# Performance work log

Measured on AMD Instinct MI355X. Metric: run time of the kernel, lower is better.

The kernel has to match this reference:

```python
import jax, jax.numpy as jnp
import numpy as np

N = 50000      # nodes
E = 1600000    # edges (avg degree 32)
NF = 128       # hidden_nf
L = 4          # n_layers
EA = 1         # edge_attr_nf


def setup_inputs() -> dict:
    key = jax.random.key(0)
    ks = jax.random.split(key, 10)
    return {
        "pos": jax.random.normal(ks[0], (N, 3), jnp.float32),
        "v": jax.random.normal(ks[1], (N, 3), jnp.float32),
        "edge_attr": jax.random.normal(ks[2], (E, EA), jnp.float32),
        # phi: Linear(1+EA -> NF), SiLU, Linear(NF -> 1, no bias), Tanh
        "phi_w1": jax.random.normal(ks[3], (L, 1 + EA, NF), jnp.float32) * 0.1,
        "phi_b1": jnp.zeros((L, NF), jnp.float32),
        "phi_w2": jax.random.normal(ks[4], (L, NF, 1), jnp.float32) * 0.001,
        # coord_mlp_vel: Linear(1 -> NF), SiLU, Linear(NF -> 1)
        "vel_w1": jax.random.normal(ks[5], (L, 1, NF), jnp.float32) * 0.1,
        "vel_b1": jnp.zeros((L, NF), jnp.float32),
        "vel_w2": jax.random.normal(ks[6], (L, NF, 1), jnp.float32) * 0.1,
        "vel_b2": jnp.zeros((L, 1), jnp.float32),
        "edge_index": jax.random.randint(ks[7], (2, E), 0, N, dtype=jnp.int64),
    }


def _layer(x, vel_norm, v, row, col, edge_attr,
           pw1, pb1, pw2, vw1, vb1, vw2, vb2):
    # edge model: gather endpoints, radial feature, per-edge MLP
    x_diff = x[row] - x[col]                                        # [E,3]
    radial = jnp.sqrt(jnp.sum(x_diff * x_diff, axis=1, keepdims=True))  # [E,1]
    e_in = jnp.concatenate([radial, edge_attr], axis=1)             # [E,1+EA]
    h = jax.nn.silu(e_in @ pw1 + pb1)                               # [E,NF]
    e_out = jnp.tanh(h @ pw2)                                       # [E,1]
    m = x_diff * e_out                                              # [E,3]
    # node model: segment mean over receiving node (row)
    agg = jax.ops.segment_sum(m, row, num_segments=N)               # [N,3]
    cnt = jax.ops.segment_sum(jnp.ones((row.shape[0], 1), x.dtype), row,
                              num_segments=N)                        # [N,1]
    x = x + agg / jnp.maximum(cnt, 1.0)
    # velocity term: x += v * coord_mlp_vel(||v||)
    phi_v = jax.nn.silu(vel_norm @ vw1 + vb1) @ vw2 + vb2           # [N,1]
    return x + v * phi_v


def reference(pos, v, edge_attr, phi_w1, phi_b1, phi_w2,
              vel_w1, vel_b1, vel_w2, vel_b2, edge_index):
    row, col = edge_index[0], edge_index[1]
    vel_norm = jnp.sqrt(jnp.sum(v * v, axis=1, keepdims=True))      # [N,1]
    x = pos
    for i in range(L):
        x = _layer(x, vel_norm, v, row, col, edge_attr,
                   phi_w1[i], phi_b1[i], phi_w2[i],
                   vel_w1[i], vel_b1[i], vel_w2[i], vel_b2[i])
    return x
```

## Files before the change

### kernel.cpp

```cpp
#include <hip/hip_runtime.h>
#include <hip/hip_fp16.h>

#define NF 128
#define NL 4

#define NR 128
#define RMAXF 16.0f
#define NA 32
#define AMINF -8.0f
#define ARANGE 16.0f
#define AQMAX 511
#define NV 512
#define VMAXF 8.0f

#define BROWS_SHIFT 7
#define BROWS 128
#define NBMAX 512
#define BCAP 4480
#define EPT 16
#define EPB 4096

struct __align__(8) Half4 { __half2 lo; __half2 hi; };

__device__ __forceinline__ float fast_sigmoid(float x) {
    float z = __builtin_amdgcn_exp2f(-1.44269504f * x);
    return __builtin_amdgcn_rcpf(1.0f + z);
}
__device__ __forceinline__ float silu(float x) { return x * fast_sigmoid(x); }

__device__ __forceinline__ float fast_tanh(float x) {
    float y = fminf(fmaxf(x, -15.0f), 15.0f);
    float e2 = __builtin_amdgcn_exp2f(2.88539008f * y);
    return (e2 - 1.0f) * __builtin_amdgcn_rcpf(e2 + 1.0f);
}

__global__ __launch_bounds__(256) void setup1_kernel(
    const float* __restrict__ pw1, const float* __restrict__ pb1,
    const float* __restrict__ pw2, const float* __restrict__ vw1,
    const float* __restrict__ vb1, const float* __restrict__ vw2,
    const float* __restrict__ vb2,
    __half* __restrict__ etabh, float* __restrict__ vtab,
    int* __restrict__ counts, int* __restrict__ cursor)
{
    int t = blockIdx.x * 256 + threadIdx.x;
    if (t < NBMAX) counts[t] = 0;
    if (t == 0) *cursor = 0;

    if (t < NL * NR * NA) {
        int l = t / (NR * NA), rem = t - l * NR * NA;
        int ri = rem / NA, ai = rem - ri * NA;
        float r = ri * (RMAXF / (NR - 1));
        float a = AMINF + ai * (ARANGE / (NA - 1));
        const float* w1r = pw1 + l * 2 * NF;
        const float* w1a = w1r + NF;
        const float* b1  = pb1 + l * NF;
        const float* w2  = pw2 + l * NF;
        float acc = 0.f;
        #pragma unroll 8
        for (int k = 0; k < NF; ++k) {
            float pre = fmaf(r, w1r[k], fmaf(a, w1a[k], b1[k]));
            acc = fmaf(silu(pre), w2[k], acc);
        }
        etabh[t] = __float2half(fast_tanh(acc));
    } else if (t < NL * NR * NA + NL * NV) {
        int u = t - NL * NR * NA;
        int l = u / NV, vi = u - l * NV;
        float vn = vi * (VMAXF / (NV - 1));
        const float* w1 = vw1 + l * NF;
        const float* b1 = vb1 + l * NF;
        const float* w2 = vw2 + l * NF;
        float acc = 0.f;
        #pragma unroll 8
        for (int k = 0; k < NF; ++k) {
            float pre = fmaf(vn, w1[k], b1[k]);
            acc = fmaf(silu(pre), w2[k], acc);
        }
        vtab[u] = acc + vb2[l];
    }
}

__global__ __launch_bounds__(256) void passA_setup2_kernel(
    const int* __restrict__ row, const int* __restrict__ col,
    const float* __restrict__ ea, int* __restrict__ counts,
    unsigned int* __restrict__ coarse, int E, int gA,
    const __half* __restrict__ etabh, Half4* __restrict__ tab,
    const float* __restrict__ pos, const float* __restrict__ v,
    const float* __restrict__ vtab,
    float4* __restrict__ x4A, float4* __restrict__ v4,
    float* __restrict__ phv, int N)
{
    int tid = threadIdx.x;
    if ((int)blockIdx.x < gA) {
        __shared__ int hist[NBMAX];
        __shared__ int base[NBMAX];
        for (int i = tid; i < NBMAX; i += 256) hist[i] = 0;
        __syncthreads();
        int e0 = blockIdx.x * EPB;
        unsigned int rec[EPT];
        int bin[EPT];
        int rank[EPT];
        #pragma unroll
        for (int k = 0; k < EPT; ++k) {
            int e = e0 + k * 256 + tid;
            bin[k] = -1;
            if (e < E) {
                int r = row[e];
                int c = col[e];
                float a = fminf(fmaxf(ea[e], AMINF), AMINF + ARANGE);
                int aq = (int)fmaf(a - AMINF, (float)AQMAX / ARANGE, 0.5f);
                bin[k]  = r >> BROWS_SHIFT;
                rec[k]  = ((unsigned int)(r & (BROWS - 1)) << 25) |
                          ((unsigned int)c << 9) | (unsigned int)aq;
                rank[k] = atomicAdd(&hist[bin[k]], 1);
            }
        }
        __syncthreads();
        for (int i = tid; i < NBMAX; i += 256) {
            int h = hist[i];
            base[i] = (h > 0) ? atomicAdd(&counts[i], h) : 0;
        }
        __syncthreads();
        #pragma unroll
        for (int k = 0; k < EPT; ++k) {
            if (bin[k] >= 0) {
                int p = base[bin[k]] + rank[k];
                if (p < BCAP) coarse[(size_t)bin[k] * BCAP + p] = rec[k];
            }
        }
    } else {
        int t = ((int)blockIdx.x - gA) * 256 + tid;
        if (t < NL * NR * NA) {
            int rem = t % (NR * NA);
            int ri = rem / NA, ai = rem - ri * NA;
            int da = (ai + 1 < NA) ? 1  : 0;
            int dr = (ri + 1 < NR) ? NA : 0;
            Half4 h;
            h.lo = __halves2half2(etabh[t], etabh[t + da]);
            h.hi = __halves2half2(etabh[t + dr], etabh[t + dr + da]);
            tab[t] = h;
        }
        if (t < N) {
            x4A[t] = make_float4(pos[t*3], pos[t*3+1], pos[t*3+2], 0.f);
            float vx = v[t*3], vy = v[t*3+1], vz = v[t*3+2];
            v4[t] = make_float4(vx, vy, vz, 0.f);
            float vn = sqrtf(vx*vx + vy*vy + vz*vz);
            float vt = fminf(vn * ((NV - 1) / VMAXF), NV - 1.0002f);
            int k0 = (int)vt; float fv = vt - (float)k0;
            #pragma unroll
            for (int l = 0; l < NL; ++l) {
                const float* vt_l = vtab + l * NV;
                phv[l * N + t] = fmaf(fv, vt_l[k0+1] - vt_l[k0], vt_l[k0]);
            }
        }
    }
}

__global__ __launch_bounds__(256) void passB_kernel(
    const unsigned int* __restrict__ coarse, const int* __restrict__ counts,
    int* __restrict__ cursor, unsigned int* __restrict__ slots,
    int2* __restrict__ sc, int N)
{
    __shared__ unsigned int recs[BCAP];
    __shared__ int hist[BROWS];
    __shared__ int excl[BROWS];
    __shared__ int cur[BROWS];
    __shared__ int cb_sh;
    int b = blockIdx.x, tid = threadIdx.x;
    int n = min(counts[b], BCAP);
    if (tid == 0) cb_sh = atomicAdd(cursor, n);
    for (int i = tid; i < n; i += 256) recs[i] = coarse[(size_t)b * BCAP + i];
    if (tid < BROWS) hist[tid] = 0;
    __syncthreads();
    for (int i = tid; i < n; i += 256) atomicAdd(&hist[recs[i] >> 25], 1);
    __syncthreads();
    if (tid < BROWS) excl[tid] = hist[tid];
    __syncthreads();
    for (int d = 1; d < BROWS; d <<= 1) {
        int vv = 0;
        if (tid < BROWS && tid >= d) vv = excl[tid - d];
        __syncthreads();
        if (tid < BROWS) excl[tid] += vv;
        __syncthreads();
    }
    int cb = cb_sh;
    if (tid < BROWS) {
        int e = excl[tid] - hist[tid];
        excl[tid] = e;
        cur[tid]  = e;
        int r = b * BROWS + tid;
        if (r < N) sc[r] = make_int2(cb + e, hist[tid]);
    }
    __syncthreads();
    for (int i = tid; i < n; i += 256) {
        unsigned int rc = recs[i];
        int p = atomicAdd(&cur[rc >> 25], 1);
        slots[cb + p] = rc & 0x01FFFFFFu;
    }
}

__global__ __launch_bounds__(256) void layer_kernel(
    const float4* __restrict__ xo, float4* __restrict__ xn4,
    float* __restrict__ xn3,
    const unsigned int* __restrict__ slots, const int2* __restrict__ sc,
    const Half4* __restrict__ tab, const float4* __restrict__ v4,
    const float* __restrict__ phv, int n)
{
    int sub = threadIdx.x & 7;
    int r = blockIdx.x * 32 + (threadIdx.x >> 3);
    if (r >= n) return;
    int2 s = sc[r];
    int m = s.y;
    float4 xr = xo[r];
    float mx = 0.f, my = 0.f, mz = 0.f;

    for (int jb = sub; jb < m; jb += 32) {
        bool p1 = (jb + 8)  < m;
        bool p2 = (jb + 16) < m;
        bool p3 = (jb + 24) < m;
        unsigned int r0 = slots[s.x + jb];
        unsigned int r1 = p1 ? slots[s.x + jb + 8]  : r0;
        unsigned int r2 = p2 ? slots[s.x + jb + 16] : r0;
        unsigned int r3 = p3 ? slots[s.x + jb + 24] : r0;
        float4 xc0 = xo[r0 >> 9];
        float4 xc1 = xo[r1 >> 9];
        float4 xc2 = xo[r2 >> 9];
        float4 xc3 = xo[r3 >> 9];

        #define EDGE(REC, XC, W) do {                                        \
            float at_ = (float)((REC) & 511u) * ((NA - 1) / (float)AQMAX);   \
            float dx_ = xr.x - (XC).x, dy_ = xr.y - (XC).y, dz_ = xr.z - (XC).z; \
            float rad_ = sqrtf(dx_*dx_ + dy_*dy_ + dz_*dz_);                 \
            float rt_ = fminf(rad_ * ((NR - 1) / RMAXF), NR - 1.0002f);      \
            int i0_ = (int)rt_; float fr_ = rt_ - (float)i0_;                \
            int j0_ = (int)at_; float fa_ = at_ - (float)j0_;                \
            Half4 p_ = tab[i0_ * NA + j0_];                                  \
            float v00_ = __low2float(p_.lo),  v01_ = __high2float(p_.lo);    \
            float v10_ = __low2float(p_.hi),  v11_ = __high2float(p_.hi);    \
            float top_ = fmaf(fa_, v01_ - v00_, v00_);                       \
            float bot_ = fmaf(fa_, v11_ - v10_, v10_);                       \
            float e_   = fmaf(fr_, bot_ - top_, top_) * (W);                 \
            mx = fmaf(dx_, e_, mx); my = fmaf(dy_, e_, my); mz = fmaf(dz_, e_, mz); \
        } while (0)

        EDGE(r0, xc0, 1.0f);
        EDGE(r1, xc1, p1 ? 1.0f : 0.0f);
        EDGE(r2, xc2, p2 ? 1.0f : 0.0f);
        EDGE(r3, xc3, p3 ? 1.0f : 0.0f);
        #undef EDGE
    }

    #pragma unroll
    for (int d = 1; d < 8; d <<= 1) {
        mx += __shfl_xor(mx, d);
        my += __shfl_xor(my, d);
        mz += __shfl_xor(mz, d);
    }
    if (sub == 0) {
        float inv = __builtin_amdgcn_rcpf(fmaxf((float)m, 1.0f));
        float4 vv = v4[r];
        float ph = phv[r];
        float ox = fmaf(mx, inv, fmaf(vv.x, ph, xr.x));
        float oy = fmaf(my, inv, fmaf(vv.y, ph, xr.y));
        float oz = fmaf(mz, inv, fmaf(vv.z, ph, xr.z));
        if (xn3) { xn3[r*3+0] = ox; xn3[r*3+1] = oy; xn3[r*3+2] = oz; }
        else     { xn4[r] = make_float4(ox, oy, oz, 0.f); }
    }
}

extern "C" void kernel_launch(void* const* d_in, const int* in_sizes, int n_in,
                              void* d_out, int out_size, void* d_ws, size_t ws_size,
                              hipStream_t stream) {
    const float* pos = (const float*)d_in[0];
    const float* v   = (const float*)d_in[1];
    const float* ea  = (const float*)d_in[2];
    const float* pw1 = (const float*)d_in[3];
    const float* pb1 = (const float*)d_in[4];
    const float* pw2 = (const float*)d_in[5];
    const float* vw1 = (const float*)d_in[6];
    const float* vb1 = (const float*)d_in[7];
    const float* vw2 = (const float*)d_in[8];
    const float* vb2 = (const float*)d_in[9];
    const int*   ei  = (const int*)d_in[10];

    const int N = in_sizes[0] / 3;
    const int E = in_sizes[10] / 2;
    const int* row = ei;
    const int* col = ei + E;
    const int nb = (N + BROWS - 1) >> BROWS_SHIFT;

    char*   ws  = (char*)d_ws;
    float4* x4A = (float4*)ws;
    float4* x4B = x4A + N;
    float4* v4  = x4B + N;
    Half4*  tab = (Half4*)(v4 + N);
    unsigned int* coarse = (unsigned int*)(tab + (size_t)NL * NR * NA);
    unsigned int* slots  = coarse + (size_t)nb * BCAP;
    int2*   sc     = (int2*)(slots + E);
    float*  phv    = (float*)(sc + N);
    __half* etabh  = (__half*)(phv + (size_t)NL * N);
    float*  vtab   = (float*)(etabh + (size_t)NL * NR * NA);
    int*    counts = (int*)(vtab + (size_t)NL * NV);
    int*    cursor = counts + NBMAX;

    float* x = (float*)d_out;
    dim3 blk(256);

    int t1 = NL * NR * NA + NL * NV;
    setup1_kernel<<<(t1 + 255)/256, blk, 0, stream>>>(
        pw1, pb1, pw2, vw1, vb1, vw2, vb2, etabh, vtab, counts, cursor);

    int gA  = (E + EPB - 1) / EPB;
    int t2  = (NL * NR * NA > N) ? NL * NR * NA : N;
    int gS2 = (t2 + 255) / 256;
    passA_setup2_kernel<<<gA + gS2, blk, 0, stream>>>(
        row, col, ea, counts, coarse, E, gA,
        etabh, tab, pos, v, vtab, x4A, v4, phv, N);

    passB_kernel<<<nb, blk, 0, stream>>>(coarse, counts, cursor, slots, sc, N);

    int gR = (N + 31) / 32;
    const size_t TSZ = (size_t)NR * NA;
    layer_kernel<<<gR, blk, 0, stream>>>(x4A, x4B, nullptr, slots, sc, tab + 0*TSZ, v4, phv + 0*(size_t)N, N);
    layer_kernel<<<gR, blk, 0, stream>>>(x4B, x4A, nullptr, slots, sc, tab + 1*TSZ, v4, phv + 1*(size_t)N, N);
    layer_kernel<<<gR, blk, 0, stream>>>(x4A, x4B, nullptr, slots, sc, tab + 2*TSZ, v4, phv + 2*(size_t)N, N);
    layer_kernel<<<gR, blk, 0, stream>>>(x4B, nullptr, x,   slots, sc, tab + 3*TSZ, v4, phv + 3*(size_t)N, N);
}
```

Measured before the change: 106.9 us.

## Pad per-row edge slots to multiples of four and load them as uint4

Pass B now rounds each row's slot count up to a multiple of four and fills the padding with a safe self-record, so each row segment starts 16-byte aligned. The layer kernel then reads four slot records per thread with one vector load instead of four scalar loads, and assigns 16 lanes per row instead of 8. Padded entries are masked with a zero weight. This costs extra slot memory and a bit more padding work, and halves the rows handled per block, which may leave lanes idle on low-degree rows.

```diff
diff --git a/kernel.cpp b/kernel.cpp
--- a/kernel.cpp
+++ b/kernel.cpp
@@ -167,13 +167,12 @@
     __shared__ int cb_sh;
     int b = blockIdx.x, tid = threadIdx.x;
     int n = min(counts[b], BCAP);
-    if (tid == 0) cb_sh = atomicAdd(cursor, n);
     for (int i = tid; i < n; i += 256) recs[i] = coarse[(size_t)b * BCAP + i];
     if (tid < BROWS) hist[tid] = 0;
     __syncthreads();
     for (int i = tid; i < n; i += 256) atomicAdd(&hist[recs[i] >> 25], 1);
     __syncthreads();
-    if (tid < BROWS) excl[tid] = hist[tid];
+    if (tid < BROWS) excl[tid] = (hist[tid] + 3) & ~3;
     __syncthreads();
     for (int d = 1; d < BROWS; d <<= 1) {
         int vv = 0;
@@ -182,13 +181,18 @@
         if (tid < BROWS) excl[tid] += vv;
         __syncthreads();
     }
+    if (tid == 0) cb_sh = atomicAdd(cursor, excl[BROWS - 1]);
+    __syncthreads();
     int cb = cb_sh;
     if (tid < BROWS) {
-        int e = excl[tid] - hist[tid];
-        excl[tid] = e;
-        cur[tid]  = e;
+        int h  = hist[tid];
+        int ha = (h + 3) & ~3;
+        int e  = excl[tid] - ha;
+        cur[tid] = e;
         int r = b * BROWS + tid;
-        if (r < N) sc[r] = make_int2(cb + e, hist[tid]);
+        if (r < N) sc[r] = make_int2(cb + e, h);
+        unsigned int saferec = ((unsigned int)min(r, N - 1) << 9);
+        for (int p = h; p < ha; ++p) slots[cb + e + p] = saferec;
     }
     __syncthreads();
     for (int i = tid; i < n; i += 256) {
@@ -205,26 +209,20 @@
     const Half4* __restrict__ tab, const float4* __restrict__ v4,
     const float* __restrict__ phv, int n)
 {
-    int sub = threadIdx.x & 7;
-    int r = blockIdx.x * 32 + (threadIdx.x >> 3);
+    int sub = threadIdx.x & 15;
+    int r = blockIdx.x * 16 + (threadIdx.x >> 4);
     if (r >= n) return;
     int2 s = sc[r];
     int m = s.y;
     float4 xr = xo[r];
     float mx = 0.f, my = 0.f, mz = 0.f;
 
-    for (int jb = sub; jb < m; jb += 32) {
-        bool p1 = (jb + 8)  < m;
-        bool p2 = (jb + 16) < m;
-        bool p3 = (jb + 24) < m;
-        unsigned int r0 = slots[s.x + jb];
-        unsigned int r1 = p1 ? slots[s.x + jb + 8]  : r0;
-        unsigned int r2 = p2 ? slots[s.x + jb + 16] : r0;
-        unsigned int r3 = p3 ? slots[s.x + jb + 24] : r0;
-        float4 xc0 = xo[r0 >> 9];
-        float4 xc1 = xo[r1 >> 9];
-        float4 xc2 = xo[r2 >> 9];
-        float4 xc3 = xo[r3 >> 9];
+    for (int kb = sub * 4; kb < m; kb += 64) {
+        uint4 q = *reinterpret_cast<const uint4*>(slots + s.x + kb);
+        float4 xc0 = xo[q.x >> 9];
+        float4 xc1 = xo[q.y >> 9];
+        float4 xc2 = xo[q.z >> 9];
+        float4 xc3 = xo[q.w >> 9];
 
         #define EDGE(REC, XC, W) do {                                        \
             float at_ = (float)((REC) & 511u) * ((NA - 1) / (float)AQMAX);   \
@@ -242,15 +240,15 @@
             mx = fmaf(dx_, e_, mx); my = fmaf(dy_, e_, my); mz = fmaf(dz_, e_, mz); \
         } while (0)
 
-        EDGE(r0, xc0, 1.0f);
-        EDGE(r1, xc1, p1 ? 1.0f : 0.0f);
-        EDGE(r2, xc2, p2 ? 1.0f : 0.0f);
-        EDGE(r3, xc3, p3 ? 1.0f : 0.0f);
+        EDGE(q.x, xc0, 1.0f);
+        EDGE(q.y, xc1, (kb + 1 < m) ? 1.0f : 0.0f);
+        EDGE(q.z, xc2, (kb + 2 < m) ? 1.0f : 0.0f);
+        EDGE(q.w, xc3, (kb + 3 < m) ? 1.0f : 0.0f);
         #undef EDGE
     }
 
     #pragma unroll
-    for (int d = 1; d < 8; d <<= 1) {
+    for (int d = 1; d < 16; d <<= 1) {
         mx += __shfl_xor(mx, d);
         my += __shfl_xor(my, d);
         mz += __shfl_xor(mz, d);
@@ -295,7 +293,7 @@
     Half4*  tab = (Half4*)(v4 + N);
     unsigned int* coarse = (unsigned int*)(tab + (size_t)NL * NR * NA);
     unsigned int* slots  = coarse + (size_t)nb * BCAP;
-    int2*   sc     = (int2*)(slots + E);
+    int2*   sc     = (int2*)(slots + (size_t)E + 4*(size_t)N + 64);
     float*  phv    = (float*)(sc + N);
     __half* etabh  = (__half*)(phv + (size_t)NL * N);
     float*  vtab   = (float*)(etabh + (size_t)NL * NR * NA);
@@ -318,7 +316,7 @@
 
     passB_kernel<<<nb, blk, 0, stream>>>(coarse, counts, cursor, slots, sc, N);
 
-    int gR = (N + 31) / 32;
+    int gR = (N + 15) / 16;
     const size_t TSZ = (size_t)NR * NA;
     layer_kernel<<<gR, blk, 0, stream>>>(x4A, x4B, nullptr, slots, sc, tab + 0*TSZ, v4, phv + 0*(size_t)N, N);
     layer_kernel<<<gR, blk, 0, stream>>>(x4B, x4A, nullptr, slots, sc, tab + 1*TSZ, v4, phv + 1*(size_t)N, N);
```

After: 99.53 us. 6.9% less time.
